# Kernel optimization log

Measured on AMD Instinct MI355X. Metric: run time of the kernel, lower is better.

## Reference

```python
import jax, jax.numpy as jnp
import numpy as np

B, S, D_IN, D_QK, D_V = 4, 4096, 1024, 64, 64

def setup_inputs() -> dict:
    key = jax.random.key(0)
    ks = jax.random.split(key, 8)
    sd = 1.0 / np.sqrt(D_IN)
    return {
        "X": jax.random.normal(ks[0], (B, S, D_IN), dtype=jnp.float32),
        "mask": jnp.ones((B, S, 1), dtype=jnp.float32),
        "Wq": jax.random.uniform(ks[1], (D_IN, D_QK), jnp.float32, -sd, sd),
        "bq": jax.random.uniform(ks[2], (D_QK,), jnp.float32, -sd, sd),
        "Wk": jax.random.uniform(ks[3], (D_IN, D_QK), jnp.float32, -sd, sd),
        "bk": jax.random.uniform(ks[4], (D_QK,), jnp.float32, -sd, sd),
        "Wv": jax.random.uniform(ks[5], (D_IN, D_V), jnp.float32, -sd, sd),
        "bv": jax.random.uniform(ks[6], (D_V,), jnp.float32, -sd, sd),
    }

def reference(X, mask, Wq, bq, Wk, bk, Wv, bv):
    # ReLU-activated projections (no head split, no 1/sqrt(d) scaling)
    q = jax.nn.relu(jnp.einsum('bsd,df->bsf', X, Wq) + bq)   # [B,S,D_QK]
    k = jax.nn.relu(jnp.einsum('bsd,df->bsf', X, Wk) + bk)   # [B,S,D_QK]
    v = jax.nn.relu(jnp.einsum('bsd,df->bsf', X, Wv) + bv)   # [B,S,D_V]
    scores = jax.nn.softmax(jnp.einsum('bqf,bkf->bqk', q, k), axis=-1)  # [B,S,S]
    return jnp.einsum('bqk,bkf->bqf', scores, v) * mask       # mask applied AFTER AV
```

## Files before the change

kernel.cpp:

```cpp
#include <hip/hip_runtime.h>


typedef short s16x8 __attribute__((ext_vector_type(8)));
typedef float fx4   __attribute__((ext_vector_type(4)));
typedef unsigned short u16x4 __attribute__((ext_vector_type(4)));

#define LOG2E 1.4426950408889634f

__device__ __forceinline__ unsigned short f2bf(float x) {
    unsigned int u = __float_as_uint(x);
    u += 0x7FFFu + ((u >> 16) & 1u);
    return (unsigned short)(u >> 16);
}
__device__ __forceinline__ float bf2f(unsigned short b) {
    return __uint_as_float(((unsigned int)b) << 16);
}

__global__ __launch_bounds__(256) void prep_w_kernel(
    const float* __restrict__ Wq, const float* __restrict__ Wk, const float* __restrict__ Wv,
    unsigned short* __restrict__ wt_hi, unsigned short* __restrict__ wt_lo)
{
    __shared__ __align__(16) unsigned short sh[64][72];
    __shared__ __align__(16) unsigned short sl[64][72];

    const int y  = blockIdx.x;
    const int kt = blockIdx.y;
    const float* W = (y == 0) ? Wq : (y == 1) ? Wk : Wv;
    const int t  = threadIdx.x;

    const int kl = t >> 2;
    const int c0 = (t & 3) * 16;
    const float* src = W + (size_t)(kt * 64 + kl) * 64 + c0;
    #pragma unroll
    for (int j = 0; j < 4; j++) {
        fx4 v = *(const fx4*)(src + j * 4);
        #pragma unroll
        for (int i = 0; i < 4; i++) {
            float x = v[i];
            unsigned short h = f2bf(x);
            unsigned short l = f2bf(x - bf2f(h));
            sh[c0 + j * 4 + i][kl] = h;
            sl[c0 + j * 4 + i][kl] = l;
        }
    }
    __syncthreads();

    const int c  = t >> 2;
    const int k0 = (t & 3) * 16;
    size_t o = (size_t)(y * 64 + c) * 1024 + kt * 64 + k0;
    *(s16x8*)(wt_hi + o)     = *(const s16x8*)&sh[c][k0];
    *(s16x8*)(wt_hi + o + 8) = *(const s16x8*)&sh[c][k0 + 8];
    *(s16x8*)(wt_lo + o)     = *(const s16x8*)&sl[c][k0];
    *(s16x8*)(wt_lo + o + 8) = *(const s16x8*)&sl[c][k0 + 8];
}

__global__ __launch_bounds__(256, 3) void proj_kernel(
    const float* __restrict__ X,
    const unsigned short* __restrict__ wt_hi, const unsigned short* __restrict__ wt_lo,
    const float* __restrict__ bq, const float* __restrict__ bk, const float* __restrict__ bv,
    unsigned short* __restrict__ q_hi, unsigned short* __restrict__ q_lo,
    unsigned short* __restrict__ k_bf, unsigned short* __restrict__ vt_g)
{
    __shared__ __align__(16) unsigned short wls[2][64][136];

    const int tid  = threadIdx.x;
    const int lane = tid & 63;
    const int w    = tid >> 6;
    const int quad = lane >> 4;
    const int l15  = lane & 15;

    const int f   = blockIdx.x;
    const int xcd = f & 7;
    const int jj  = f >> 3;
    const int y   = jj % 3;
    const int m0  = ((jj / 3) * 8 + xcd) * 64;

    const int row = m0 + w * 16 + l15;
    const float* xbase = X + (size_t)row * 1024;

    const int wcol = tid >> 2;
    const int wk0  = (tid & 3) * 32;
    const size_t wgb = (size_t)(y * 64 + wcol) * 1024 + wk0;

    s16x8 wrh[4], wrl[4];
    #pragma unroll
    for (int i = 0; i < 4; i++) {
        wrh[i] = *(const s16x8*)(wt_hi + wgb + i * 8);
        wrl[i] = *(const s16x8*)(wt_lo + wgb + i * 8);
    }
    fx4 xc[2][2];
    #pragma unroll
    for (int ks = 0; ks < 2; ks++) {
        xc[ks][0] = *(const fx4*)(xbase + ks * 32 + quad * 8);
        xc[ks][1] = *(const fx4*)(xbase + ks * 32 + quad * 8 + 4);
    }

    fx4 acc[4];
    #pragma unroll
    for (int nt = 0; nt < 4; nt++) acc[nt] = (fx4){0.f, 0.f, 0.f, 0.f};

    for (int ch = 0; ch < 8; ch++) {
        if (ch) __syncthreads();
        #pragma unroll
        for (int i = 0; i < 4; i++) {
            *(s16x8*)&wls[0][wcol][wk0 + i * 8] = wrh[i];
            *(s16x8*)&wls[1][wcol][wk0 + i * 8] = wrl[i];
        }
        __syncthreads();
        if (ch < 7) {
            #pragma unroll
            for (int i = 0; i < 4; i++) {
                wrh[i] = *(const s16x8*)(wt_hi + wgb + (ch + 1) * 128 + i * 8);
                wrl[i] = *(const s16x8*)(wt_lo + wgb + (ch + 1) * 128 + i * 8);
            }
        }

        #pragma unroll
        for (int kk = 0; kk < 2; kk++) {
            const int kc = ch * 2 + kk;
            fx4 xn[2][2];
            if (kc < 15) {
                #pragma unroll
                for (int ks = 0; ks < 2; ks++) {
                    xn[ks][0] = *(const fx4*)(xbase + (kc + 1) * 64 + ks * 32 + quad * 8);
                    xn[ks][1] = *(const fx4*)(xbase + (kc + 1) * 64 + ks * 32 + quad * 8 + 4);
                }
            }
            s16x8 ah[2], al[2];
            #pragma unroll
            for (int ks = 0; ks < 2; ks++) {
                #pragma unroll
                for (int j = 0; j < 2; j++) {
                    fx4 v = xc[ks][j];
                    #pragma unroll
                    for (int i = 0; i < 4; i++) {
                        unsigned short h = f2bf(v[i]);
                        ah[ks][j * 4 + i] = (short)h;
                        al[ks][j * 4 + i] = (short)f2bf(v[i] - bf2f(h));
                    }
                }
            }
            #pragma unroll
            for (int nt = 0; nt < 4; nt++) {
                #pragma unroll
                for (int ks = 0; ks < 2; ks++) {
                    const int ko = kk * 64 + ks * 32 + quad * 8;
                    s16x8 bh = *(const s16x8*)&wls[0][nt * 16 + l15][ko];
                    s16x8 bl = *(const s16x8*)&wls[1][nt * 16 + l15][ko];
                    acc[nt] = __builtin_amdgcn_mfma_f32_16x16x32_bf16(ah[ks], bh, acc[nt], 0, 0, 0);
                    acc[nt] = __builtin_amdgcn_mfma_f32_16x16x32_bf16(ah[ks], bl, acc[nt], 0, 0, 0);
                    acc[nt] = __builtin_amdgcn_mfma_f32_16x16x32_bf16(al[ks], bh, acc[nt], 0, 0, 0);
                }
            }
            #pragma unroll
            for (int ks = 0; ks < 2; ks++) {
                xc[ks][0] = xn[ks][0];
                xc[ks][1] = xn[ks][1];
            }
        }
    }
    __syncthreads();

    const float* bias = (y == 0) ? bq : (y == 1) ? bk : bv;
    const int b   = m0 >> 12;
    const int s0b = m0 & 4095;
    unsigned short* vtr = &wls[0][0][0];

    #pragma unroll
    for (int nt = 0; nt < 4; nt++) {
        int col = nt * 16 + l15;
        float bb = bias[col];
        int rloc = w * 16 + quad * 4;
        #pragma unroll
        for (int r = 0; r < 4; r++) {
            float v = acc[nt][r] + bb;
            v = fmaxf(v, 0.f);
            size_t grow = (size_t)(m0 + rloc + r);
            if (y == 0) {
                unsigned short h = f2bf(v);
                unsigned short l = f2bf(v - bf2f(h));
                q_hi[grow * 64 + col] = h;
                q_lo[grow * 64 + col] = l;
            } else if (y == 1) {
                k_bf[grow * 64 + col] = f2bf(v);
            } else {
                vtr[col * 72 + rloc + r] = f2bf(v);
            }
        }
    }
    if (y == 2) {
        __syncthreads();
        int rowd = tid >> 2;
        int off  = (tid & 3) * 16;
        s16x8 v0 = *(const s16x8*)&vtr[rowd * 72 + off];
        s16x8 v1 = *(const s16x8*)&vtr[rowd * 72 + off + 8];
        *(s16x8*)(vt_g + (size_t)(b * 64 + rowd) * 4096 + s0b + off)     = v0;
        *(s16x8*)(vt_g + (size_t)(b * 64 + rowd) * 4096 + s0b + off + 8) = v1;
    }
}

__global__ __launch_bounds__(256, 6) void attn_kernel(
    const unsigned short* __restrict__ q_hi, const unsigned short* __restrict__ q_lo,
    const unsigned short* __restrict__ k_bf, const unsigned short* __restrict__ vt_g,
    unsigned short* __restrict__ pOb, float* __restrict__ pL)
{
    __shared__ __align__(16) unsigned short kt[64][72];
    __shared__ __align__(16) unsigned short vt[64][72];
    __shared__ __align__(16) unsigned short pt[4][16][40];

    const int tid  = threadIdx.x;
    const int lane = tid & 63;
    const int w    = tid >> 6;
    const int quad = lane >> 4;
    const int l15  = lane & 15;
    const int ck   = blockIdx.y;
    const int b    = blockIdx.z;
    const int q0   = blockIdx.x * 64;

    const size_t qoff = ((size_t)b * 4096 + q0 + w * 16 + l15) * 64 + quad * 8;
    s16x8 qh0 = *(const s16x8*)(q_hi + qoff);
    s16x8 qh1 = *(const s16x8*)(q_hi + qoff + 32);
    s16x8 ql0 = *(const s16x8*)(q_lo + qoff);
    s16x8 ql1 = *(const s16x8*)(q_lo + qoff + 32);

    fx4 accO[4];
    #pragma unroll
    for (int nt = 0; nt < 4; nt++) accO[nt] = (fx4){0.f, 0.f, 0.f, 0.f};
    float lsum[4] = {0.f, 0.f, 0.f, 0.f};

    const unsigned short* kgb = k_bf + (size_t)b * 4096 * 64;
    const unsigned short* vgb = vt_g + (size_t)b * 64 * 4096;

    const int srow = tid >> 3;
    const int soff = (tid & 7) * 8;

    for (int it = ck * 8; it < ck * 8 + 8; it++) {
        const unsigned short* kg = kgb + (size_t)it * 4096;
        #pragma unroll
        for (int i = 0; i < 2; i++) {
            int row = srow + i * 32;
            *(s16x8*)&kt[row][soff] = *(const s16x8*)(kg + (size_t)row * 64 + soff);
            *(s16x8*)&vt[row][soff] = *(const s16x8*)(vgb + (size_t)row * 4096 + it * 64 + soff);
        }
        __syncthreads();

        #pragma unroll
        for (int kh = 0; kh < 2; kh++) {
            #pragma unroll
            for (int nt2 = 0; nt2 < 2; nt2++) {
                int key = kh * 32 + nt2 * 16 + l15;
                s16x8 k0 = *(const s16x8*)&kt[key][quad * 8];
                s16x8 k1 = *(const s16x8*)&kt[key][32 + quad * 8];
                fx4 sc = (fx4){0.f, 0.f, 0.f, 0.f};
                sc = __builtin_amdgcn_mfma_f32_16x16x32_bf16(qh0, k0, sc, 0, 0, 0);
                sc = __builtin_amdgcn_mfma_f32_16x16x32_bf16(ql0, k0, sc, 0, 0, 0);
                sc = __builtin_amdgcn_mfma_f32_16x16x32_bf16(qh1, k1, sc, 0, 0, 0);
                sc = __builtin_amdgcn_mfma_f32_16x16x32_bf16(ql1, k1, sc, 0, 0, 0);
                #pragma unroll
                for (int r = 0; r < 4; r++) {
                    float p = __builtin_amdgcn_exp2f(sc[r] * LOG2E);
                    unsigned short pb = f2bf(p);
                    lsum[r] += bf2f(pb);
                    pt[w][quad * 4 + r][nt2 * 16 + l15] = pb;
                }
            }
            s16x8 pa = *(const s16x8*)&pt[w][l15][quad * 8];
            #pragma unroll
            for (int nt = 0; nt < 4; nt++) {
                s16x8 vf = *(const s16x8*)&vt[nt * 16 + l15][kh * 32 + quad * 8];
                accO[nt] = __builtin_amdgcn_mfma_f32_16x16x32_bf16(pa, vf, accO[nt], 0, 0, 0);
            }
        }
        __syncthreads();
    }

    #pragma unroll
    for (int r = 0; r < 4; r++) {
        float v = lsum[r];
        #pragma unroll
        for (int o = 1; o < 16; o <<= 1) v += __shfl_xor(v, o);
        lsum[r] = v;
    }
    #pragma unroll
    for (int r = 0; r < 4; r++) {
        int qrow = q0 + w * 16 + quad * 4 + r;
        size_t grow = (size_t)b * 4096 + qrow;
        #pragma unroll
        for (int nt = 0; nt < 4; nt++)
            pOb[((size_t)ck * 16384 + grow) * 64 + nt * 16 + l15] = f2bf(accO[nt][r]);
        if (l15 == 0)
            pL[(size_t)ck * 16384 + grow] = lsum[r];
    }
}

__global__ __launch_bounds__(256) void combine_kernel(
    const unsigned short* __restrict__ pOb, const float* __restrict__ pL,
    const float* __restrict__ mask, float* __restrict__ out)
{
    int idx = blockIdx.x * 256 + threadIdx.x;
    int q  = idx >> 4;
    int dg = idx & 15;
    fx4 s = (fx4){0.f, 0.f, 0.f, 0.f};
    float l = 0.f;
    #pragma unroll
    for (int c = 0; c < 8; c++) {
        u16x4 h = *(const u16x4*)(pOb + ((size_t)c * 16384 + q) * 64 + dg * 4);
        s.x += bf2f(h.x);
        s.y += bf2f(h.y);
        s.z += bf2f(h.z);
        s.w += bf2f(h.w);
        l += pL[(size_t)c * 16384 + q];
    }
    float scale = mask[q] / l;
    *(fx4*)(out + (size_t)q * 64 + dg * 4) = s * scale;
}

extern "C" void kernel_launch(void* const* d_in, const int* in_sizes, int n_in,
                              void* d_out, int out_size, void* d_ws, size_t ws_size,
                              hipStream_t stream)
{
    const float* X    = (const float*)d_in[0];
    const float* mask = (const float*)d_in[1];
    const float* Wq   = (const float*)d_in[2];
    const float* bq   = (const float*)d_in[3];
    const float* Wk   = (const float*)d_in[4];
    const float* bk   = (const float*)d_in[5];
    const float* Wv   = (const float*)d_in[6];
    const float* bv   = (const float*)d_in[7];
    float* out = (float*)d_out;

    char* ws = (char*)d_ws;
    unsigned short* q_hi  = (unsigned short*)(ws);
    unsigned short* q_lo  = (unsigned short*)(ws + (size_t)(2u << 20));
    unsigned short* k_bf  = (unsigned short*)(ws + (size_t)(4u << 20));
    unsigned short* vt_g  = (unsigned short*)(ws + (size_t)(6u << 20));
    unsigned short* wt_hi = (unsigned short*)(ws + (size_t)(8u << 20));
    unsigned short* wt_lo = (unsigned short*)(ws + (size_t)(8u << 20) + 393216);
    unsigned short* pOb   = (unsigned short*)(ws + (size_t)(9u << 20));
    float*          pL    = (float*)(ws + (size_t)(25u << 20));

    hipLaunchKernelGGL(prep_w_kernel, dim3(3, 16), dim3(256), 0, stream,
                       Wq, Wk, Wv, wt_hi, wt_lo);
    hipLaunchKernelGGL(proj_kernel, dim3(768), dim3(256), 0, stream,
                       X, wt_hi, wt_lo, bq, bk, bv, q_hi, q_lo, k_bf, vt_g);
    hipLaunchKernelGGL(attn_kernel, dim3(64, 8, 4), dim3(256), 0, stream,
                       q_hi, q_lo, k_bf, vt_g, pOb, pL);
    hipLaunchKernelGGL(combine_kernel, dim3(1024), dim3(256), 0, stream,
                       pOb, pL, mask, out);
}
```

Baseline: 180.2 us.

## Use single fp16 MFMA for projections and prefetch K/V tiles in attention

The projection GEMM drops the split-bf16 (hi/lo) emulation of three MFMAs per step and uses a single fp16 MFMA, with weights and X converted to fp16. Weight chunks grow to 256 columns per stage, and the occupancy hint rises from 3 to 4 blocks per CU. The attention kernel now register-prefetches the next K/V tile while computing on the current one, which removes one barrier per iteration. The projection now does about a third of its MFMA work, but fp16 has fewer mantissa bits than the old hi/lo scheme and a narrower range, so accuracy may drop.

```diff
diff --git a/kernel.cpp b/kernel.cpp
--- a/kernel.cpp
+++ b/kernel.cpp
@@ -2,6 +2,7 @@
 
 
 typedef short s16x8 __attribute__((ext_vector_type(8)));
+typedef _Float16 f16x8 __attribute__((ext_vector_type(8)));
 typedef float fx4   __attribute__((ext_vector_type(4)));
 typedef unsigned short u16x4 __attribute__((ext_vector_type(4)));
 
@@ -18,10 +19,9 @@
 
 __global__ __launch_bounds__(256) void prep_w_kernel(
     const float* __restrict__ Wq, const float* __restrict__ Wk, const float* __restrict__ Wv,
-    unsigned short* __restrict__ wt_hi, unsigned short* __restrict__ wt_lo)
-{
-    __shared__ __align__(16) unsigned short sh[64][72];
-    __shared__ __align__(16) unsigned short sl[64][72];
+    _Float16* __restrict__ wt_h)
+{
+    __shared__ __align__(16) _Float16 sh[64][72];
 
     const int y  = blockIdx.x;
     const int kt = blockIdx.y;
@@ -35,33 +35,26 @@
     for (int j = 0; j < 4; j++) {
         fx4 v = *(const fx4*)(src + j * 4);
         #pragma unroll
-        for (int i = 0; i < 4; i++) {
-            float x = v[i];
-            unsigned short h = f2bf(x);
-            unsigned short l = f2bf(x - bf2f(h));
-            sh[c0 + j * 4 + i][kl] = h;
-            sl[c0 + j * 4 + i][kl] = l;
-        }
+        for (int i = 0; i < 4; i++)
+            sh[c0 + j * 4 + i][kl] = (_Float16)v[i];
     }
     __syncthreads();
 
     const int c  = t >> 2;
     const int k0 = (t & 3) * 16;
     size_t o = (size_t)(y * 64 + c) * 1024 + kt * 64 + k0;
-    *(s16x8*)(wt_hi + o)     = *(const s16x8*)&sh[c][k0];
-    *(s16x8*)(wt_hi + o + 8) = *(const s16x8*)&sh[c][k0 + 8];
-    *(s16x8*)(wt_lo + o)     = *(const s16x8*)&sl[c][k0];
-    *(s16x8*)(wt_lo + o + 8) = *(const s16x8*)&sl[c][k0 + 8];
-}
-
-__global__ __launch_bounds__(256, 3) void proj_kernel(
+    *(f16x8*)(wt_h + o)     = *(const f16x8*)&sh[c][k0];
+    *(f16x8*)(wt_h + o + 8) = *(const f16x8*)&sh[c][k0 + 8];
+}
+
+__global__ __launch_bounds__(256, 4) void proj_kernel(
     const float* __restrict__ X,
-    const unsigned short* __restrict__ wt_hi, const unsigned short* __restrict__ wt_lo,
+    const _Float16* __restrict__ wt_h,
     const float* __restrict__ bq, const float* __restrict__ bk, const float* __restrict__ bv,
     unsigned short* __restrict__ q_hi, unsigned short* __restrict__ q_lo,
     unsigned short* __restrict__ k_bf, unsigned short* __restrict__ vt_g)
 {
-    __shared__ __align__(16) unsigned short wls[2][64][136];
+    __shared__ __align__(16) _Float16 wls[64][264];
 
     const int tid  = threadIdx.x;
     const int lane = tid & 63;
@@ -79,15 +72,14 @@
     const float* xbase = X + (size_t)row * 1024;
 
     const int wcol = tid >> 2;
-    const int wk0  = (tid & 3) * 32;
+    const int wk0  = (tid & 3) * 64;
     const size_t wgb = (size_t)(y * 64 + wcol) * 1024 + wk0;
 
-    s16x8 wrh[4], wrl[4];
-    #pragma unroll
-    for (int i = 0; i < 4; i++) {
-        wrh[i] = *(const s16x8*)(wt_hi + wgb + i * 8);
-        wrl[i] = *(const s16x8*)(wt_lo + wgb + i * 8);
-    }
+    f16x8 wr[8];
+    #pragma unroll
+    for (int i = 0; i < 8; i++)
+        wr[i] = *(const f16x8*)(wt_h + wgb + i * 8);
+
     fx4 xc[2][2];
     #pragma unroll
     for (int ks = 0; ks < 2; ks++) {
@@ -99,25 +91,21 @@
     #pragma unroll
     for (int nt = 0; nt < 4; nt++) acc[nt] = (fx4){0.f, 0.f, 0.f, 0.f};
 
-    for (int ch = 0; ch < 8; ch++) {
+    for (int ch = 0; ch < 4; ch++) {
         if (ch) __syncthreads();
         #pragma unroll
-        for (int i = 0; i < 4; i++) {
-            *(s16x8*)&wls[0][wcol][wk0 + i * 8] = wrh[i];
-            *(s16x8*)&wls[1][wcol][wk0 + i * 8] = wrl[i];
-        }
+        for (int i = 0; i < 8; i++)
+            *(f16x8*)&wls[wcol][wk0 + i * 8] = wr[i];
         __syncthreads();
-        if (ch < 7) {
-            #pragma unroll
-            for (int i = 0; i < 4; i++) {
-                wrh[i] = *(const s16x8*)(wt_hi + wgb + (ch + 1) * 128 + i * 8);
-                wrl[i] = *(const s16x8*)(wt_lo + wgb + (ch + 1) * 128 + i * 8);
-            }
-        }
-
-        #pragma unroll
-        for (int kk = 0; kk < 2; kk++) {
-            const int kc = ch * 2 + kk;
+        if (ch < 3) {
+            #pragma unroll
+            for (int i = 0; i < 8; i++)
+                wr[i] = *(const f16x8*)(wt_h + wgb + (ch + 1) * 256 + i * 8);
+        }
+
+        #pragma unroll
+        for (int kk = 0; kk < 4; kk++) {
+            const int kc = ch * 4 + kk;
             fx4 xn[2][2];
             if (kc < 15) {
                 #pragma unroll
@@ -126,30 +114,23 @@
                     xn[ks][1] = *(const fx4*)(xbase + (kc + 1) * 64 + ks * 32 + quad * 8 + 4);
                 }
             }
-            s16x8 ah[2], al[2];
-            #pragma unroll
-            for (int ks = 0; ks < 2; ks++) {
+            f16x8 ah[2];
+            #pragma unroll
+            for (int ks = 0; ks < 2; ks++)
                 #pragma unroll
                 for (int j = 0; j < 2; j++) {
                     fx4 v = xc[ks][j];
                     #pragma unroll
-                    for (int i = 0; i < 4; i++) {
-                        unsigned short h = f2bf(v[i]);
-                        ah[ks][j * 4 + i] = (short)h;
-                        al[ks][j * 4 + i] = (short)f2bf(v[i] - bf2f(h));
-                    }
+                    for (int i = 0; i < 4; i++)
+                        ah[ks][j * 4 + i] = (_Float16)v[i];
                 }
-            }
             #pragma unroll
             for (int nt = 0; nt < 4; nt++) {
                 #pragma unroll
                 for (int ks = 0; ks < 2; ks++) {
                     const int ko = kk * 64 + ks * 32 + quad * 8;
-                    s16x8 bh = *(const s16x8*)&wls[0][nt * 16 + l15][ko];
-                    s16x8 bl = *(const s16x8*)&wls[1][nt * 16 + l15][ko];
-                    acc[nt] = __builtin_amdgcn_mfma_f32_16x16x32_bf16(ah[ks], bh, acc[nt], 0, 0, 0);
-                    acc[nt] = __builtin_amdgcn_mfma_f32_16x16x32_bf16(ah[ks], bl, acc[nt], 0, 0, 0);
-                    acc[nt] = __builtin_amdgcn_mfma_f32_16x16x32_bf16(al[ks], bh, acc[nt], 0, 0, 0);
+                    f16x8 bh = *(const f16x8*)&wls[nt * 16 + l15][ko];
+                    acc[nt] = __builtin_amdgcn_mfma_f32_16x16x32_f16(ah[ks], bh, acc[nt], 0, 0, 0);
                 }
             }
             #pragma unroll
@@ -164,7 +145,7 @@
     const float* bias = (y == 0) ? bq : (y == 1) ? bk : bv;
     const int b   = m0 >> 12;
     const int s0b = m0 & 4095;
-    unsigned short* vtr = &wls[0][0][0];
+    unsigned short* vtr = (unsigned short*)&wls[0][0];
 
     #pragma unroll
     for (int nt = 0; nt < 4; nt++) {
@@ -234,15 +215,36 @@
     const int srow = tid >> 3;
     const int soff = (tid & 7) * 8;
 
-    for (int it = ck * 8; it < ck * 8 + 8; it++) {
-        const unsigned short* kg = kgb + (size_t)it * 4096;
+    s16x8 kr[2], vr[2];
+    {
+        const unsigned short* kg = kgb + (size_t)(ck * 8) * 4096;
         #pragma unroll
         for (int i = 0; i < 2; i++) {
             int row = srow + i * 32;
-            *(s16x8*)&kt[row][soff] = *(const s16x8*)(kg + (size_t)row * 64 + soff);
-            *(s16x8*)&vt[row][soff] = *(const s16x8*)(vgb + (size_t)row * 4096 + it * 64 + soff);
+            kr[i] = *(const s16x8*)(kg + (size_t)row * 64 + soff);
+            vr[i] = *(const s16x8*)(vgb + (size_t)row * 4096 + (ck * 8) * 64 + soff);
+        }
+    }
+
+    for (int i2 = 0; i2 < 8; i2++) {
+        const int it = ck * 8 + i2;
+        if (i2) __syncthreads();
+        #pragma unroll
+        for (int i = 0; i < 2; i++) {
+            int row = srow + i * 32;
+            *(s16x8*)&kt[row][soff] = kr[i];
+            *(s16x8*)&vt[row][soff] = vr[i];
         }
         __syncthreads();
+        if (i2 < 7) {
+            const unsigned short* kg = kgb + (size_t)(it + 1) * 4096;
+            #pragma unroll
+            for (int i = 0; i < 2; i++) {
+                int row = srow + i * 32;
+                kr[i] = *(const s16x8*)(kg + (size_t)row * 64 + soff);
+                vr[i] = *(const s16x8*)(vgb + (size_t)row * 4096 + (it + 1) * 64 + soff);
+            }
+        }
 
         #pragma unroll
         for (int kh = 0; kh < 2; kh++) {
@@ -271,7 +273,6 @@
                 accO[nt] = __builtin_amdgcn_mfma_f32_16x16x32_bf16(pa, vf, accO[nt], 0, 0, 0);
             }
         }
-        __syncthreads();
     }
 
     #pragma unroll
@@ -334,15 +335,14 @@
     unsigned short* q_lo  = (unsigned short*)(ws + (size_t)(2u << 20));
     unsigned short* k_bf  = (unsigned short*)(ws + (size_t)(4u << 20));
     unsigned short* vt_g  = (unsigned short*)(ws + (size_t)(6u << 20));
-    unsigned short* wt_hi = (unsigned short*)(ws + (size_t)(8u << 20));
-    unsigned short* wt_lo = (unsigned short*)(ws + (size_t)(8u << 20) + 393216);
+    _Float16*       wt_h  = (_Float16*)(ws + (size_t)(8u << 20));
     unsigned short* pOb   = (unsigned short*)(ws + (size_t)(9u << 20));
     float*          pL    = (float*)(ws + (size_t)(25u << 20));
 
     hipLaunchKernelGGL(prep_w_kernel, dim3(3, 16), dim3(256), 0, stream,
-                       Wq, Wk, Wv, wt_hi, wt_lo);
+                       Wq, Wk, Wv, wt_h);
     hipLaunchKernelGGL(proj_kernel, dim3(768), dim3(256), 0, stream,
-                       X, wt_hi, wt_lo, bq, bk, bv, q_hi, q_lo, k_bf, vt_g);
+                       X, wt_h, bq, bk, bv, q_hi, q_lo, k_bf, vt_g);
     hipLaunchKernelGGL(attn_kernel, dim3(64, 8, 4), dim3(256), 0, stream,
                        q_hi, q_lo, k_bf, vt_g, pOb, pL);
     hipLaunchKernelGGL(combine_kernel, dim3(1024), dim3(256), 0, stream,
```

After: 177.7 us. About the same (-1.4%).
